# Performance work log

Hardware: AMD Instinct MI355X
Metric: run time of the kernel (lower is better)

The kernel has to match this reference:

```python
import jax, jax.numpy as jnp
import numpy as np

NL, H, PD, NH, NB = 4, 256, 64, 4, 65
B, L, AA = 2, 384, 48
DH = H // NH
MAX_REL = 32


def _ln(x, g, b):
    m = x.mean(-1, keepdims=True)
    v = ((x - m) ** 2).mean(-1, keepdims=True)
    return (x - m) * jax.lax.rsqrt(v + 1e-5) * g + b


def setup_inputs() -> dict:
    key = jax.random.key(0)
    ks = iter(jax.random.split(key, 64))
    w = lambda *s: jax.random.normal(next(ks), s, jnp.float32) * 0.02
    return dict(
        x=jax.random.normal(next(ks), (B, L, AA), jnp.float32),
        rp_w=w(AA, H), rp_b=jnp.zeros((H,), jnp.float32),
        pos_embed=w(L, H),
        pii_w=w(H, PD), pii_b=jnp.zeros((PD,), jnp.float32),
        pij_w=w(H, PD), pij_b=jnp.zeros((PD,), jnp.float32),
        rel_emb=w(2 * MAX_REL + 2, PD),
        ln_seq_g=jnp.ones((NL, H), jnp.float32), ln_seq_b=jnp.zeros((NL, H), jnp.float32),
        ln_pair_g=jnp.ones((NL, PD), jnp.float32), ln_pair_b=jnp.zeros((NL, PD), jnp.float32),
        pb_w=w(NL, PD, NH),
        in_w=w(NL, H, 3 * H), in_b=jnp.zeros((NL, 3 * H), jnp.float32),
        out_w=w(NL, H, H), out_b=jnp.zeros((NL, H), jnp.float32),
        ff_ln_g=jnp.ones((NL, H), jnp.float32), ff_ln_b=jnp.zeros((NL, H), jnp.float32),
        ff_w1=w(NL, H, 4 * H), ff_b1=jnp.zeros((NL, 4 * H), jnp.float32),
        ff_w2=w(NL, 4 * H, H), ff_b2=jnp.zeros((NL, H), jnp.float32),
        pu_ln_g=jnp.ones((NL, PD), jnp.float32), pu_ln_b=jnp.zeros((NL, PD), jnp.float32),
        pu_w1=w(NL, PD, PD), pu_b1=jnp.zeros((NL, PD), jnp.float32),
        pu_w2=w(NL, PD, PD), pu_b2=jnp.zeros((NL, PD), jnp.float32),
        outer_w=w(NL, 2 * H, PD), outer_b=jnp.zeros((NL, PD), jnp.float32),
        dh_ln_g=jnp.ones((PD,), jnp.float32), dh_ln_b=jnp.zeros((PD,), jnp.float32),
        dh_w1=w(PD, PD), dh_b1=jnp.zeros((PD,), jnp.float32),
        dh_w2=w(PD, NB), dh_b2=jnp.zeros((NB,), jnp.float32),
    )


def reference(x, rp_w, rp_b, pos_embed, pii_w, pii_b, pij_w, pij_b, rel_emb,
              ln_seq_g, ln_seq_b, ln_pair_g, ln_pair_b, pb_w, in_w, in_b,
              out_w, out_b, ff_ln_g, ff_ln_b, ff_w1, ff_b1, ff_w2, ff_b2,
              pu_ln_g, pu_ln_b, pu_w1, pu_b1, pu_w2, pu_b2, outer_w, outer_b,
              dh_ln_g, dh_ln_b, dh_w1, dh_b1, dh_w2, dh_b2):
    Bx, Lx, _ = x.shape
    gelu = lambda t: jax.nn.gelu(t, approximate=False)  # torch nn.GELU default (erf)
    h = x @ rp_w + rp_b + pos_embed[:Lx][None]
    # pair init: outer sum of two linear projections + clipped rel-pos embedding
    pair = (h @ pii_w + pii_b)[:, :, None, :] + (h @ pij_w + pij_b)[:, None, :, :]
    idx = jnp.arange(Lx)
    rel = jnp.clip(idx[None, :] - idx[:, None], -MAX_REL, MAX_REL) + MAX_REL  # (L,L)
    pair = pair + rel_emb[rel][None]
    for i in range(NL):
        seq_n = _ln(h, ln_seq_g[i], ln_seq_b[i])
        bias = _ln(pair, ln_pair_g[i], ln_pair_b[i]) @ pb_w[i]  # (B,L,L,NH)
        mask = bias.mean(axis=(0, 3))  # torch: permute->reshape(B*NH,L,L)->mean(0)
        qkv = seq_n @ in_w[i] + in_b[i]
        q, k, v = jnp.split(qkv, 3, axis=-1)
        q = q.reshape(Bx, Lx, NH, DH)
        k = k.reshape(Bx, Lx, NH, DH)
        v = v.reshape(Bx, Lx, NH, DH)
        scores = jnp.einsum('blhd,bmhd->bhlm', q, k) / float(np.sqrt(DH)) + mask
        attn = jax.nn.softmax(scores, axis=-1)
        o = jnp.einsum('bhlm,bmhd->blhd', attn, v).reshape(Bx, Lx, H)
        h = h + o @ out_w[i] + out_b[i]
        h = h + gelu(_ln(h, ff_ln_g[i], ff_ln_b[i]) @ ff_w1[i] + ff_b1[i]) @ ff_w2[i] + ff_b2[i]
        # outer_proj(cat([h_i, h_j])) == h@W[:H] outer-summed with h@W[H:]
        oi = h @ outer_w[i][:H]
        oj = h @ outer_w[i][H:]
        outer = oi[:, :, None, :] + oj[:, None, :, :] + outer_b[i]  # (B,L,L,PD)
        pair = pair + gelu(_ln(outer, pu_ln_g[i], pu_ln_b[i]) @ pu_w1[i] + pu_b1[i]) @ pu_w2[i] + pu_b2[i]
    logits = gelu(_ln(pair, dh_ln_g, dh_ln_b) @ dh_w1 + dh_b1) @ dh_w2 + dh_b2
    return (logits + jnp.swapaxes(logits, 1, 2)) / 2.0
```

## Files before the change

### kernel.cpp

```cpp
#include <hip/hip_runtime.h>
#include <math.h>

#define LSEQ 384
#define HD 256
#define PDIM 64
#define NHEAD 4
#define NBINS 65
#define BATCH 2
#define NTT (LSEQ / 16)
#define NTRI (NTT * (NTT + 1) / 2)

typedef __attribute__((ext_vector_type(8))) short bf16x8;
typedef __attribute__((ext_vector_type(16))) float f32x16;
typedef __attribute__((ext_vector_type(4))) float f32x4;
typedef __attribute__((ext_vector_type(4))) unsigned u32x4;
typedef __attribute__((ext_vector_type(4))) short s16x4;
#define MFMA32(a, b, c) __builtin_amdgcn_mfma_f32_32x32x16_bf16(a, b, c, 0, 0, 0)

template<int CTRL, int RMASK>
__device__ __forceinline__ float dpp_sum_step(float v) {
    int x = __builtin_amdgcn_update_dpp(0, __float_as_int(v), CTRL, RMASK, 0xf, true);
    return v + __int_as_float(x);
}
template<int CTRL, int RMASK>
__device__ __forceinline__ float dpp_max_step(float v) {
// ... 49 lines not shown
        float rb = b - __uint_as_float(hp & 0xffff0000u);
        h[j] = hp;
        l[j] = cvt_pk_bf(ra, rb);
    }
}
__device__ __forceinline__ bf16x8 as_bf(u32x4 x) {
    union { u32x4 u; bf16x8 b; } c; c.u = x; return c.b;
}
__device__ __forceinline__ bf16x8 ld8(const short* p) {
    s16x4 a = *(const s16x4*)p;
    s16x4 b = *(const s16x4*)(p + 4);
    bf16x8 r;
    r[0] = a[0]; r[1] = a[1]; r[2] = a[2]; r[3] = a[3];
    r[4] = b[0]; r[5] = b[1]; r[6] = b[2]; r[7] = b[3];
    return r;
}

__global__ void k_h_init(const float* __restrict__ x, const float* __restrict__ rp_w,
                         const float* __restrict__ rp_b, const float* __restrict__ pos,
                         float* __restrict__ h) {
    __shared__ float xs[48];
    int row = blockIdx.x;
    int l = row % LSEQ;
    int t = threadIdx.x;
    if (t < 48) xs[t] = x[row * 48 + t];
    __syncthreads();
    float acc = rp_b[t] + pos[l * HD + t];
#pragma unroll 8
    for (int a = 0; a < 48; ++a) acc += xs[a] * rp_w[a * HD + t];
    h[row * HD + t] = acc;
// ... 11 lines not shown
    __syncthreads();
    int col = t & 63;
    const float* w = (t < 64) ? wA : wB;
    const float* bias = (t < 64) ? bA : bB;
    float acc = bias ? bias[col] : 0.0f;
#pragma unroll 8
    for (int a = 0; a < HD; ++a) acc += hs[a] * w[a * PDIM + col];
    if (center) {
        float mean = wsum(acc) * (1.0f / PDIM);
        acc -= mean;
    }
    float* p = (t < 64) ? pA : pB;
    p[row * PDIM + col] = acc;
}

__global__ void __launch_bounds__(64) k_pair_init2(
    const float* __restrict__ pi, const float* __restrict__ pj,
    const float* __restrict__ rel_emb, const float* __restrict__ gpb,
    const float* __restrict__ cbv, float* __restrict__ pair,
    float* __restrict__ mask_out) {
    __shared__ __align__(16) float pt[32][65];
    int blk = blockIdx.x;
    int row = blk / 12, seg = blk % 12;
    int b = row / LSEQ, i = row % LSEQ;
    int t = threadIdx.x;
    int pl = t & 31, hq = t >> 5;
    int j0 = seg * 32;
    float piv = pi[row * 64 + t];
    const float* pjb = pj + ((size_t)b * LSEQ + j0) * 64;
#pragma unroll 8
    for (int j = 0; j < 32; ++j) {
        int r = j0 + j - i; r = r < -32 ? -32 : (r > 32 ? 32 : r); r += 32;
        pt[j][t] = piv + pjb[j * 64 + t] + rel_emb[r * 64 + t];
    }
    __syncthreads();
    float4* dst4 = (float4*)(pair + ((size_t)row * LSEQ + j0) * 64);
    for (int n = t; n < 512; n += 64) {
        int r2 = n >> 4, c4 = (n & 15) << 2;
        float4 g4 = { pt[r2][c4], pt[r2][c4 + 1], pt[r2][c4 + 2], pt[r2][c4 + 3] };
        dst4[n] = g4;
    }
    float vv[32];
    float sv = 0.0f;
#pragma unroll
    for (int c = 0; c < 32; ++c) { vv[c] = pt[pl][hq * 32 + c]; sv += vv[c]; }
    sv += __shfl_xor(sv, 32);
    float mean = sv * (1.0f / PDIM);
    float sd2 = 0.0f, sdg = 0.0f;
#pragma unroll
    for (int c = 0; c < 32; ++c) {
        float d = vv[c] - mean;
        sd2 = fmaf(d, d, sd2);
        sdg = fmaf(d, gpb[hq * 32 + c], sdg);
    }
    sd2 += __shfl_xor(sd2, 32);
    sdg += __shfl_xor(sdg, 32);
// ... 189 lines not shown
    if (lane == 0) red[4 + w] = ws;
    __syncthreads();
    float inv = 1.0f / (red[4] + red[5] + red[6] + red[7]);
    int d = t & 63, gq = t >> 6;
    float part = 0.0f;
    for (int m = gq * 96; m < (gq + 1) * 96; ++m)
        part += sc[m] * qkv[((size_t)(b * LSEQ + m)) * 768 + 512 + nh * 64 + d];
    op[gq][d] = part;
    __syncthreads();
    if (t < 64) {
        float ov = (op[0][t] + op[1][t] + op[2][t] + op[3][t]) * inv;
        o[((size_t)(b * LSEQ + l)) * HD + nh * 64 + t] = ov;
    }
}

template<bool DIST>
__global__ void __launch_bounds__(256) k_pair_upd(
    const float* __restrict__ ojc,
    const float* __restrict__ oic,
    const unsigned short* __restrict__ w1hT, const unsigned short* __restrict__ w1lT,
    const float* __restrict__ b1p,
    const unsigned short* __restrict__ w2hT, const unsigned short* __restrict__ w2lT,
    const float* __restrict__ b2, float* __restrict__ pair,
    const float* __restrict__ gpb, const float* __restrict__ cbv,
    float* __restrict__ mask_out,
    const unsigned short* __restrict__ dw1h, const unsigned short* __restrict__ dw1l,
    const float* __restrict__ db1p,
    const unsigned short* __restrict__ dw2h, const unsigned short* __restrict__ dw2l,
    const float* __restrict__ w2c, const float* __restrict__ db2,
    float* __restrict__ outg) {
    __shared__ __align__(16) char smem[DIST ? 33344 : 17472];
    short (*lw)[64][68] = (short (*)[64][68])smem;
    int blk = blockIdx.x;
    int row = blk / 3, seg = blk % 3;
    int b = row / LSEQ;
    int t = threadIdx.x;
    int wave = t >> 6, lane = t & 63;
    int pl = lane & 31, hq = lane >> 5;
    int jj = wave * 32 + pl;
    int p = seg * 128 + jj;
    const float* ojr = ojc + ((size_t)b * LSEQ + p) * 64;
    const float* oir = oic + (size_t)row * 64;
    float* prp = pair + ((size_t)row * LSEQ + p) * 64;

#define STAGE2(srcA, srcB) \
    for (int idx = t; idx < 2048; idx += 256) { \
        int rr2 = idx >> 5, cc2 = (idx & 31) * 2; \
        *(unsigned*)&lw[0][rr2][cc2] = *(const unsigned*)(srcA + rr2 * 64 + cc2); \
        *(unsigned*)&lw[1][rr2][cc2] = *(const unsigned*)(srcB + rr2 * 64 + cc2); \
    }

    float v[32];
    {
        const f32x4* a4 = (const f32x4*)ojr;
        const f32x4* c4 = (const f32x4*)oir;
#pragma unroll
        for (int s = 0; s < 4; ++s) {
            f32x4 a = a4[4 * s + 2 * hq], aa = a4[4 * s + 2 * hq + 1];
            f32x4 c = c4[4 * s + 2 * hq], cc = c4[4 * s + 2 * hq + 1];
#pragma unroll
            for (int j = 0; j < 4; ++j) {
                v[8 * s + j] = a[j] + c[j];
                v[8 * s + 4 + j] = aa[j] + cc[j];
            }
        }
    }
    STAGE2(w1hT, w1lT)

    float ss = 0.0f;
#pragma unroll
    for (int i = 0; i < 32; ++i) ss = fmaf(v[i], v[i], ss);
    ss += __shfl_xor(ss, 32);
    float rs = rsqrtf(ss * (1.0f / PDIM) + 1e-5f);
#pragma unroll
    for (int i = 0; i < 32; ++i) v[i] *= rs;
    u32x4 zh[4], zl[4];
#pragma unroll
    for (int s = 0; s < 4; ++s) pack8(v + 8 * s, zh[s], zl[s]);

    const f32x4* b14 = (const f32x4*)b1p;
    f32x4 bi0[4], bi1[4];
#pragma unroll
// ... 11 lines not shown
    for (int s = 0; s < 4; ++s) {
        int ko = 16 * s + 8 * hq;
        bf16x8 a0h = ld8(&lw[0][pl][ko]);
        bf16x8 a0l = ld8(&lw[1][pl][ko]);
        bf16x8 a1h = ld8(&lw[0][32 + pl][ko]);
        bf16x8 a1l = ld8(&lw[1][32 + pl][ko]);
        bf16x8 zhs = as_bf(zh[s]), zls = as_bf(zl[s]);
        acc0 = MFMA32(a0h, zhs, acc0);
        acc0 = MFMA32(a0h, zls, acc0);
        acc0 = MFMA32(a0l, zhs, acc0);
        acc1 = MFMA32(a1h, zhs, acc1);
        acc1 = MFMA32(a1h, zls, acc1);
        acc1 = MFMA32(a1l, zhs, acc1);
    }
    __syncthreads();
    STAGE2(w2hT, w2lT)

    float u0[16], u1[16];
#pragma unroll
    for (int r = 0; r < 16; ++r) { u0[r] = gelu_erf(acc0[r]); u1[r] = gelu_erf(acc1[r]); }

    f32x4 r0[4], r1[4], q0[4], q1[4];
    {
        const f32x4* pr4 = (const f32x4*)prp;
        const f32x4* b24 = (const f32x4*)b2;
#pragma unroll
        for (int g = 0; g < 4; ++g) {
            r0[g] = pr4[2 * g + hq];
            r1[g] = pr4[8 + 2 * g + hq];
            q0[g] = b24[2 * g + hq];
            q1[g] = b24[8 + 2 * g + hq];
        }
    }

    float rA0[4], rB0[4], rA1[4], rB1[4];
#pragma unroll
    for (int i = 0; i < 4; ++i) {
        rA0[i] = __shfl_xor(hq ? u0[i] : u0[4 + i], 32);
        rB0[i] = __shfl_xor(hq ? u0[8 + i] : u0[12 + i], 32);
        rA1[i] = __shfl_xor(hq ? u1[i] : u1[4 + i], 32);
        rB1[i] = __shfl_xor(hq ? u1[8 + i] : u1[12 + i], 32);
    }
    u32x4 uh[4], ul[4];
#pragma unroll
    for (int s = 0; s < 4; ++s) {
        int tt = s >> 1, q = s & 1;
// ... 22 lines not shown
    for (int s = 0; s < 4; ++s) {
        int ko = 16 * s + 8 * hq;
        bf16x8 a0h = ld8(&lw[0][pl][ko]);
        bf16x8 a0l = ld8(&lw[1][pl][ko]);
        bf16x8 a1h = ld8(&lw[0][32 + pl][ko]);
        bf16x8 a1l = ld8(&lw[1][32 + pl][ko]);
        bf16x8 uhs = as_bf(uh[s]), uls = as_bf(ul[s]);
        c0 = MFMA32(a0h, uhs, c0);
        c0 = MFMA32(a0h, uls, c0);
        c0 = MFMA32(a0l, uhs, c0);
        c1 = MFMA32(a1h, uhs, c1);
        c1 = MFMA32(a1h, uls, c1);
        c1 = MFMA32(a1l, uhs, c1);
    }

    if constexpr (!DIST) {
        const f32x4* gp4 = (const f32x4*)gpb;
        f32x4 gp0[4], gp1[4];
#pragma unroll
        for (int g = 0; g < 4; ++g) { gp0[g] = gp4[2 * g + hq]; gp1[g] = gp4[8 + 2 * g + hq]; }
        float sv = 0.0f;
#pragma unroll
        for (int r = 0; r < 16; ++r) sv += c0[r] + c1[r];
        sv += __shfl_xor(sv, 32);
        float mean = sv * (1.0f / PDIM);
        float sd2 = 0.0f, sdg = 0.0f;
#pragma unroll 4
        for (int r = 0; r < 16; ++r) {
            int g = r >> 2, i = r & 3;
            float d0 = c0[r] - mean, d1 = c1[r] - mean;
            sd2 = fmaf(d0, d0, sd2);
            sd2 = fmaf(d1, d1, sd2);
            sdg = fmaf(d0, gp0[g][i], sdg);
            sdg = fmaf(d1, gp1[g][i], sdg);
        }
        sd2 += __shfl_xor(sd2, 32);
        sdg += __shfl_xor(sdg, 32);
        float rsv = rsqrtf(sd2 * (1.0f / PDIM) + 1e-5f);
        float dot = rsv * sdg + cbv[0];
        if (hq == 0)
            atomicAdd(mask_out + (row % LSEQ) * LSEQ + p, dot * (1.0f / (BATCH * NHEAD)));
        f32x4* pw4 = (f32x4*)prp;
#pragma unroll
        for (int g = 0; g < 4; ++g) {
            f32x4 s0, s1;
#pragma unroll
            for (int i = 0; i < 4; ++i) { s0[i] = c0[4 * g + i]; s1[i] = c1[4 * g + i]; }
            pw4[2 * g + hq] = s0;
            pw4[8 + 2 * g + hq] = s1;
        }
    } else {
        float ra[4], rb[4], rc[4], rd[4];
#pragma unroll
        for (int i = 0; i < 4; ++i) {
            ra[i] = __shfl_xor(hq ? c0[i] : c0[4 + i], 32);
            rb[i] = __shfl_xor(hq ? c0[8 + i] : c0[12 + i], 32);
            rc[i] = __shfl_xor(hq ? c1[i] : c1[4 + i], 32);
            rd[i] = __shfl_xor(hq ? c1[8 + i] : c1[12 + i], 32);
        }
        float v2[32];
#pragma unroll
        for (int i = 0; i < 4; ++i) {
            v2[i]      = hq ? ra[i] : c0[i];
            v2[4 + i]  = hq ? c0[4 + i] : ra[i];
            v2[8 + i]  = hq ? rb[i] : c0[8 + i];
            v2[12 + i] = hq ? c0[12 + i] : rb[i];
            v2[16 + i] = hq ? rc[i] : c1[i];
            v2[20 + i] = hq ? c1[4 + i] : rc[i];
            v2[24 + i] = hq ? rd[i] : c1[8 + i];
            v2[28 + i] = hq ? c1[12 + i] : rd[i];
        }
        __syncthreads();
        STAGE2(dw1h, dw1l)

        float sm = 0.0f;
#pragma unroll
        for (int i = 0; i < 32; ++i) sm += v2[i];
        sm += __shfl_xor(sm, 32);
        float mean = sm * (1.0f / PDIM);
        float ss2 = 0.0f;
#pragma unroll
        for (int i = 0; i < 32; ++i) { v2[i] -= mean; ss2 = fmaf(v2[i], v2[i], ss2); }
        ss2 += __shfl_xor(ss2, 32);
        float rs2 = rsqrtf(ss2 * (1.0f / PDIM) + 1e-5f);
#pragma unroll
        for (int i = 0; i < 32; ++i) v2[i] *= rs2;
#pragma unroll
        for (int s = 0; s < 4; ++s) pack8(v2 + 8 * s, zh[s], zl[s]);

        const f32x4* d14 = (const f32x4*)db1p;
        const f32x4* d24 = (const f32x4*)db2;
        const f32x4* wc4 = (const f32x4*)w2c;
        f32x4 di0[4], di1[4], e0[4], e1[4], wc0[4], wc1[4];
#pragma unroll
        for (int g = 0; g < 4; ++g) {
            di0[g] = d14[2 * g + hq]; di1[g] = d14[8 + 2 * g + hq];
            e0[g] = d24[2 * g + hq];  e1[g] = d24[8 + 2 * g + hq];
            wc0[g] = wc4[2 * g + hq]; wc1[g] = wc4[8 + 2 * g + hq];
        }
        __syncthreads();

#pragma unroll
        for (int r = 0; r < 16; ++r) {
            acc0[r] = di0[r >> 2][r & 3];
            acc1[r] = di1[r >> 2][r & 3];
        }
#pragma unroll
        for (int s = 0; s < 4; ++s) {
            int ko = 16 * s + 8 * hq;
            bf16x8 a0h = ld8(&lw[0][pl][ko]);
            bf16x8 a0l = ld8(&lw[1][pl][ko]);
            bf16x8 a1h = ld8(&lw[0][32 + pl][ko]);
            bf16x8 a1l = ld8(&lw[1][32 + pl][ko]);
            bf16x8 zhs = as_bf(zh[s]), zls = as_bf(zl[s]);
            acc0 = MFMA32(a0h, zhs, acc0);
            acc0 = MFMA32(a0h, zls, acc0);
            acc0 = MFMA32(a0l, zhs, acc0);
            acc1 = MFMA32(a1h, zhs, acc1);
            acc1 = MFMA32(a1h, zls, acc1);
            acc1 = MFMA32(a1l, zhs, acc1);
        }
        __syncthreads();
        STAGE2(dw2h, dw2l)

        float p64 = 0.0f;
#pragma unroll
        for (int r = 0; r < 16; ++r) {
            int g = r >> 2, i = r & 3;
            u0[r] = gelu_erf(acc0[r]);
            u1[r] = gelu_erf(acc1[r]);
            p64 = fmaf(u0[r], wc0[g][i], p64);
            p64 = fmaf(u1[r], wc1[g][i], p64);
        }
        p64 += __shfl_xor(p64, 32);
#pragma unroll
        for (int i = 0; i < 4; ++i) {
            rA0[i] = __shfl_xor(hq ? u0[i] : u0[4 + i], 32);
            rB0[i] = __shfl_xor(hq ? u0[8 + i] : u0[12 + i], 32);
            rA1[i] = __shfl_xor(hq ? u1[i] : u1[4 + i], 32);
            rB1[i] = __shfl_xor(hq ? u1[8 + i] : u1[12 + i], 32);
        }
#pragma unroll
        for (int s = 0; s < 4; ++s) {
            int tt = s >> 1, q = s & 1;
            float fg[8];
#pragma unroll
            for (int i = 0; i < 4; ++i) {
                float own_f = q ? (tt ? u1[8 + i] : u0[8 + i]) : (tt ? u1[i] : u0[i]);
                float own_s = q ? (tt ? u1[12 + i] : u0[12 + i]) : (tt ? u1[4 + i] : u0[4 + i]);
                float rcv   = q ? (tt ? rB1[i] : rB0[i]) : (tt ? rA1[i] : rA0[i]);
                fg[i]     = hq ? rcv : own_f;
                fg[4 + i] = hq ? own_s : rcv;
            }
            pack8(fg, uh[s], ul[s]);
        }
        __syncthreads();

#pragma unroll
        for (int r = 0; r < 16; ++r) {
            c0[r] = e0[r >> 2][r & 3];
            c1[r] = e1[r >> 2][r & 3];
        }
#pragma unroll
        for (int s = 0; s < 4; ++s) {
            int ko = 16 * s + 8 * hq;
            bf16x8 a0h = ld8(&lw[0][pl][ko]);
            bf16x8 a0l = ld8(&lw[1][pl][ko]);
            bf16x8 a1h = ld8(&lw[0][32 + pl][ko]);
            bf16x8 a1l = ld8(&lw[1][32 + pl][ko]);
            bf16x8 uhs = as_bf(uh[s]), uls = as_bf(ul[s]);
            c0 = MFMA32(a0h, uhs, c0);
            c0 = MFMA32(a0h, uls, c0);
            c0 = MFMA32(a0l, uhs, c0);
            c1 = MFMA32(a1h, uhs, c1);
            c1 = MFMA32(a1h, uls, c1);
            c1 = MFMA32(a1l, uhs, c1);
        }
        __syncthreads();
        float (*pt)[65] = (float (*)[65])smem;
#pragma unroll
        for (int r = 0; r < 16; ++r) {
            int rr = (r & 3) + 8 * (r >> 2) + 4 * hq;
            pt[jj][rr] = c0[r];
            pt[jj][32 + rr] = c1[r];
        }
        if (hq == 0) pt[jj][64] = p64 + db2[64];
        __syncthreads();
        float4* dst = (float4*)(outg + ((size_t)row * LSEQ + seg * 128) * NBINS);
        const float4* srcl = (const float4*)&pt[0][0];
        for (int n = t; n < 128 * NBINS / 4; n += 256) dst[n] = srcl[n];
    }
#undef STAGE2
}

__global__ void k_sym(float* __restrict__ out) {
    int u = blockIdx.x;
    int b = 0;
    if (u >= NTRI) { b = 1; u -= NTRI; }
    int lt = 0, rem = NTT;
    while (u >= rem) { u -= rem; ++lt; --rem; }
    int mt = lt + u;
    int t = threadIdx.x;
    int g = t >> 6, lane = t & 63;
    float* ob = out + (size_t)b * LSEQ * LSEQ * NBINS;
    for (int e = g; e < 256; e += 4) {
        int i = e >> 4, j = e & 15;
        if (lt == mt && j < i) continue;
        size_t ia = ((size_t)(lt * 16 + i) * LSEQ + (mt * 16 + j)) * NBINS;
        size_t ib = ((size_t)(mt * 16 + j) * LSEQ + (lt * 16 + i)) * NBINS;
        for (int k = lane; k < NBINS; k += 64) {
            float a = ob[ia + k], c = ob[ib + k];
            float vv = 0.5f * (a + c);
            ob[ia + k] = vv;
            if (ia != ib) ob[ib + k] = vv;
        }
    }
}

extern "C" void kernel_launch(void* const* d_in, const int* in_sizes, int n_in,
                              void* d_out, int out_size, void* d_ws, size_t ws_size,
                              hipStream_t stream) {
    const float* x        = (const float*)d_in[0];
    const float* rp_w     = (const float*)d_in[1];
    const float* rp_b     = (const float*)d_in[2];
    const float* pos      = (const float*)d_in[3];
    const float* pii_w    = (const float*)d_in[4];
    const float* pii_b    = (const float*)d_in[5];
    const float* pij_w    = (const float*)d_in[6];
    const float* pij_b    = (const float*)d_in[7];
// ... 27 lines not shown
    const float* dh_b1    = (const float*)d_in[35];
    const float* dh_w2    = (const float*)d_in[36];
    const float* dh_b2    = (const float*)d_in[37];
    float* outp = (float*)d_out;

    float* W = (float*)d_ws;
    float* h    = W;  W += BATCH * LSEQ * HD;
    float* sn   = W;  W += BATCH * LSEQ * HD;
    float* qkv  = W;  W += BATCH * LSEQ * 3 * HD;
    float* ob   = W;  W += BATCH * LSEQ * HD;
    float* mid  = W;  W += BATCH * LSEQ * 4 * HD;
    float* maskA= W;  W += LSEQ * LSEQ;
    float* maskB= W;  W += LSEQ * LSEQ;
    float* poi  = W;  W += BATCH * LSEQ * PDIM;
    float* poj  = W;  W += BATCH * LSEQ * PDIM;
    float* b1p  = W;  W += 5 * 64;
    float* w2c  = W;  W += 64;
    float* gpb  = W;  W += 4 * 64;
    float* cbv  = W;  W += 64;
    unsigned short* w1hT = (unsigned short*)W;  W += 5 * 2048;
    unsigned short* w1lT = (unsigned short*)W;  W += 5 * 2048;
    unsigned short* w2hT = (unsigned short*)W;  W += 5 * 2048;
    unsigned short* w2lT = (unsigned short*)W;  W += 5 * 2048;
    unsigned short* qwT_h = (unsigned short*)W;  W += 4 * 196608 / 2;
    unsigned short* qwT_l = (unsigned short*)W;  W += 4 * 196608 / 2;
    unsigned short* owT_h = (unsigned short*)W;  W += 4 * 65536 / 2;
    unsigned short* owT_l = (unsigned short*)W;  W += 4 * 65536 / 2;
    unsigned short* f1T_h = (unsigned short*)W;  W += 4 * 262144 / 2;
    unsigned short* f1T_l = (unsigned short*)W;  W += 4 * 262144 / 2;
    unsigned short* f2T_h = (unsigned short*)W;  W += 4 * 262144 / 2;
    unsigned short* f2T_l = (unsigned short*)W;  W += 4 * 262144 / 2;
    float* pair = W;  W += (size_t)BATCH * LSEQ * LSEQ * PDIM;

    const int rows = BATCH * LSEQ;

    k_prep<<<5, 64, 0, stream>>>(pu_ln_g, pu_ln_b, pu_w1, pu_b1, pu_w2,
                                 dh_ln_g, dh_ln_b, dh_w1, dh_b1, dh_w2,
                                 w1hT, w1lT, w2hT, w2lT, b1p, w2c);
    k_maskprep<<<4, 64, 0, stream>>>(ln_pair_g, ln_pair_b, pb_w, gpb, cbv);
    k_split_T<<<4 * 4 * 12, 256, 0, stream>>>(in_w,  qwT_h, qwT_l, 256, 768,  4, 12, 196608, 196608);
    k_split_T<<<4 * 4 * 4,  256, 0, stream>>>(out_w, owT_h, owT_l, 256, 256,  4, 4,  65536,  65536);
    k_split_T<<<4 * 4 * 16, 256, 0, stream>>>(ff_w1, f1T_h, f1T_l, 256, 1024, 4, 16, 262144, 262144);
    k_split_T<<<4 * 16 * 4, 256, 0, stream>>>(ff_w2, f2T_h, f2T_l, 1024, 256, 16, 4, 262144, 262144);
    k_h_init<<<rows, 256, 0, stream>>>(x, rp_w, rp_b, pos, h);
    k_proj2<<<rows, 128, 0, stream>>>(h, pii_w, pij_w, pii_b, pij_b, 0, poi, poj);
    hipMemsetAsync(maskA, 0, LSEQ * LSEQ * sizeof(float), stream);
    k_pair_init2<<<rows * 12, 64, 0, stream>>>(poi, poj, rel_emb, gpb, cbv, pair, maskA);

    float* mcur = maskA;
    float* mnext = maskB;
    for (int i = 0; i < 4; ++i) {
        k_ln_seq<<<rows, 256, 0, stream>>>(h, ln_seq_g + i * HD, ln_seq_b + i * HD, sn);
        k_gemm<false><<<576, 64, 0, stream>>>(sn, qwT_h + i * 196608, qwT_l + i * 196608,
                                              in_b + i * 768, nullptr, qkv, 256, 768);
        k_attn<<<BATCH * NHEAD * LSEQ, 256, 0, stream>>>(qkv, mcur, ob);
        k_gemm<false><<<192, 64, 0, stream>>>(ob, owT_h + i * 65536, owT_l + i * 65536,
                                              out_b + i * 256, h, h, 256, 256);
        k_ln_seq<<<rows, 256, 0, stream>>>(h, ff_ln_g + i * HD, ff_ln_b + i * HD, sn);
        k_gemm<true><<<768, 64, 0, stream>>>(sn, f1T_h + i * 262144, f1T_l + i * 262144,
                                             ff_b1 + i * 1024, nullptr, mid, 256, 1024);
        k_gemm<false><<<192, 64, 0, stream>>>(mid, f2T_h + i * 262144, f2T_l + i * 262144,
                                              ff_b2 + i * 256, h, h, 1024, 256);
        k_proj2<<<rows, 128, 0, stream>>>(h, outer_w + i * 2 * HD * PDIM,
                                          outer_w + i * 2 * HD * PDIM + HD * PDIM,
                                          outer_b + i * PDIM, nullptr, 1, poi, poj);
        if (i < 3) {
            hipMemsetAsync(mnext, 0, LSEQ * LSEQ * sizeof(float), stream);
            k_pair_upd<false><<<rows * 3, 256, 0, stream>>>(
                poj, poi,
                w1hT + i * 4096, w1lT + i * 4096, b1p + i * 64,
                w2hT + i * 4096, w2lT + i * 4096, pu_b2 + i * PDIM, pair,
                gpb + (i + 1) * 64, cbv + (i + 1), mnext,
                nullptr, nullptr, nullptr, nullptr, nullptr, nullptr, nullptr, nullptr);
            float* tmp = mcur; mcur = mnext; mnext = tmp;
        } else {
            k_pair_upd<true><<<rows * 3, 256, 0, stream>>>(
                poj, poi,
                w1hT + 3 * 4096, w1lT + 3 * 4096, b1p + 3 * 64,
                w2hT + 3 * 4096, w2lT + 3 * 4096, pu_b2 + 3 * PDIM, pair,
                nullptr, nullptr, nullptr,
                w1hT + 4 * 4096, w1lT + 4 * 4096, b1p + 4 * 64,
                w2hT + 4 * 4096, w2lT + 4 * 4096, w2c, dh_b2, outp);
        }
    }

    k_sym<<<2 * NTRI, 256, 0, stream>>>(outp);
}
```

Before: 1.050 ms.

## Fuse pair init into first update and symmetrize inside final distance kernel

The initial pair tensor is no longer written by the init kernel. The first pair-update pass rebuilds it on the fly from the projections and relative embeddings, so one full pair write and read is skipped. The last layer's update and distance head move into a new kernel that computes each (i,j) and (j,i) cell pair together, averages them, and writes both transposed output tiles. This removes the separate symmetrization kernel and its read-modify-write over the output, but doubles per-block MLP work for the final layer and uses a triangular tile mapping with scattered writes.

```diff
diff --git a/kernel.cpp b/kernel.cpp
--- a/kernel.cpp
+++ b/kernel.cpp
@@ -7,8 +7,6 @@
 #define NHEAD 4
 #define NBINS 65
 #define BATCH 2
-#define NTT (LSEQ / 16)
-#define NTRI (NTT * (NTT + 1) / 2)
 
 typedef __attribute__((ext_vector_type(8))) short bf16x8;
 typedef __attribute__((ext_vector_type(16))) float f32x16;
@@ -88,6 +86,16 @@
     r[0] = a[0]; r[1] = a[1]; r[2] = a[2]; r[3] = a[3];
     r[4] = b[0]; r[5] = b[1]; r[6] = b[2]; r[7] = b[3];
     return r;
+}
+
+__device__ __forceinline__ void stage_w(short (*lw)[64][68], int t,
+                                        const unsigned short* __restrict__ srcA,
+                                        const unsigned short* __restrict__ srcB) {
+    for (int idx = t; idx < 2048; idx += 256) {
+        int rr2 = idx >> 5, cc2 = (idx & 31) * 2;
+        *(unsigned*)&lw[0][rr2][cc2] = *(const unsigned*)(srcA + rr2 * 64 + cc2);
+        *(unsigned*)&lw[1][rr2][cc2] = *(const unsigned*)(srcB + rr2 * 64 + cc2);
+    }
 }
 
 __global__ void k_h_init(const float* __restrict__ x, const float* __restrict__ rp_w,
@@ -129,11 +137,10 @@
     p[row * PDIM + col] = acc;
 }
 
-__global__ void __launch_bounds__(64) k_pair_init2(
+__global__ void __launch_bounds__(64) k_mask0(
     const float* __restrict__ pi, const float* __restrict__ pj,
     const float* __restrict__ rel_emb, const float* __restrict__ gpb,
-    const float* __restrict__ cbv, float* __restrict__ pair,
-    float* __restrict__ mask_out) {
+    const float* __restrict__ cbv, float* __restrict__ mask_out) {
     __shared__ __align__(16) float pt[32][65];
     int blk = blockIdx.x;
     int row = blk / 12, seg = blk % 12;
@@ -149,12 +156,6 @@
         pt[j][t] = piv + pjb[j * 64 + t] + rel_emb[r * 64 + t];
     }
     __syncthreads();
-    float4* dst4 = (float4*)(pair + ((size_t)row * LSEQ + j0) * 64);
-    for (int n = t; n < 512; n += 64) {
-        int r2 = n >> 4, c4 = (n & 15) << 2;
-        float4 g4 = { pt[r2][c4], pt[r2][c4 + 1], pt[r2][c4 + 2], pt[r2][c4 + 3] };
-        dst4[n] = g4;
-    }
     float vv[32];
     float sv = 0.0f;
 #pragma unroll
@@ -374,7 +375,7 @@
     }
 }
 
-template<bool DIST>
+template<bool INIT>
 __global__ void __launch_bounds__(256) k_pair_upd(
     const float* __restrict__ ojc,
     const float* __restrict__ oic,
@@ -384,12 +385,9 @@
     const float* __restrict__ b2, float* __restrict__ pair,
     const float* __restrict__ gpb, const float* __restrict__ cbv,
     float* __restrict__ mask_out,
-    const unsigned short* __restrict__ dw1h, const unsigned short* __restrict__ dw1l,
-    const float* __restrict__ db1p,
-    const unsigned short* __restrict__ dw2h, const unsigned short* __restrict__ dw2l,
-    const float* __restrict__ w2c, const float* __restrict__ db2,
-    float* __restrict__ outg) {
-    __shared__ __align__(16) char smem[DIST ? 33344 : 17472];
+    const float* __restrict__ ipi, const float* __restrict__ ipj,
+    const float* __restrict__ rel) {
+    __shared__ __align__(16) char smem[17472];
     short (*lw)[64][68] = (short (*)[64][68])smem;
     int blk = blockIdx.x;
     int row = blk / 3, seg = blk % 3;
@@ -403,13 +401,6 @@
     const float* oir = oic + (size_t)row * 64;
     float* prp = pair + ((size_t)row * LSEQ + p) * 64;
 
-#define STAGE2(srcA, srcB) \
-    for (int idx = t; idx < 2048; idx += 256) { \
-        int rr2 = idx >> 5, cc2 = (idx & 31) * 2; \
-        *(unsigned*)&lw[0][rr2][cc2] = *(const unsigned*)(srcA + rr2 * 64 + cc2); \
-        *(unsigned*)&lw[1][rr2][cc2] = *(const unsigned*)(srcB + rr2 * 64 + cc2); \
-    }
-
     float v[32];
     {
         const f32x4* a4 = (const f32x4*)ojr;
@@ -425,7 +416,7 @@
             }
         }
     }
-    STAGE2(w1hT, w1lT)
+    stage_w(lw, t, w1hT, w1lT);
 
     float ss = 0.0f;
 #pragma unroll
@@ -467,7 +458,7 @@
         acc1 = MFMA32(a1l, zhs, acc1);
     }
     __syncthreads();
-    STAGE2(w2hT, w2lT)
+    stage_w(lw, t, w2hT, w2lT);
 
     float u0[16], u1[16];
 #pragma unroll
@@ -475,14 +466,29 @@
 
     f32x4 r0[4], r1[4], q0[4], q1[4];
     {
-        const f32x4* pr4 = (const f32x4*)prp;
         const f32x4* b24 = (const f32x4*)b2;
-#pragma unroll
-        for (int g = 0; g < 4; ++g) {
-            r0[g] = pr4[2 * g + hq];
-            r1[g] = pr4[8 + 2 * g + hq];
-            q0[g] = b24[2 * g + hq];
-            q1[g] = b24[8 + 2 * g + hq];
+        if constexpr (INIT) {
+            int l = row % LSEQ;
+            int rr_ = p - l; rr_ = rr_ < -32 ? -32 : (rr_ > 32 ? 32 : rr_); rr_ += 32;
+            const f32x4* i4 = (const f32x4*)(ipi + (size_t)row * 64);
+            const f32x4* j4 = (const f32x4*)(ipj + ((size_t)b * LSEQ + p) * 64);
+            const f32x4* e4 = (const f32x4*)(rel + rr_ * 64);
+#pragma unroll
+            for (int g = 0; g < 4; ++g) {
+                r0[g] = i4[2 * g + hq] + j4[2 * g + hq] + e4[2 * g + hq];
+                r1[g] = i4[8 + 2 * g + hq] + j4[8 + 2 * g + hq] + e4[8 + 2 * g + hq];
+                q0[g] = b24[2 * g + hq];
+                q1[g] = b24[8 + 2 * g + hq];
+            }
+        } else {
+            const f32x4* pr4 = (const f32x4*)prp;
+#pragma unroll
+            for (int g = 0; g < 4; ++g) {
+                r0[g] = pr4[2 * g + hq];
+                r1[g] = pr4[8 + 2 * g + hq];
+                q0[g] = b24[2 * g + hq];
+                q1[g] = b24[8 + 2 * g + hq];
+            }
         }
     }
 
@@ -535,7 +541,7 @@
         c1 = MFMA32(a1l, uhs, c1);
     }
 
-    if constexpr (!DIST) {
+    {
         const f32x4* gp4 = (const f32x4*)gpb;
         f32x4 gp0[4], gp1[4];
 #pragma unroll
@@ -561,179 +567,344 @@
         float dot = rsv * sdg + cbv[0];
         if (hq == 0)
             atomicAdd(mask_out + (row % LSEQ) * LSEQ + p, dot * (1.0f / (BATCH * NHEAD)));
-        f32x4* pw4 = (f32x4*)prp;
+    }
+    f32x4* pw4 = (f32x4*)prp;
+#pragma unroll
+    for (int g = 0; g < 4; ++g) {
+        f32x4 s0, s1;
+#pragma unroll
+        for (int i = 0; i < 4; ++i) { s0[i] = c0[4 * g + i]; s1[i] = c1[4 * g + i]; }
+        pw4[2 * g + hq] = s0;
+        pw4[8 + 2 * g + hq] = s1;
+    }
+}
+
+__device__ __forceinline__ void dist_cell(
+    int t, int pl, int hq,
+    const float* __restrict__ oiR, const float* __restrict__ ojC,
+    const float* __restrict__ prp, short (*lw)[64][68],
+    const unsigned short* __restrict__ w1hT, const unsigned short* __restrict__ w1lT,
+    const float* __restrict__ b1p,
+    const unsigned short* __restrict__ w2hT, const unsigned short* __restrict__ w2lT,
+    const float* __restrict__ b2,
+    const unsigned short* __restrict__ dw1h, const unsigned short* __restrict__ dw1l,
+    const float* __restrict__ db1p,
+    const unsigned short* __restrict__ dw2h, const unsigned short* __restrict__ dw2l,
+    const float* __restrict__ w2c, const float* __restrict__ db2,
+    f32x16& c0o, f32x16& c1o, float& p64o) {
+    __syncthreads();
+    float v[32];
+    {
+        const f32x4* a4 = (const f32x4*)ojC;
+        const f32x4* c4 = (const f32x4*)oiR;
+#pragma unroll
+        for (int s = 0; s < 4; ++s) {
+            f32x4 a = a4[4 * s + 2 * hq], aa = a4[4 * s + 2 * hq + 1];
+            f32x4 c = c4[4 * s + 2 * hq], cc = c4[4 * s + 2 * hq + 1];
+#pragma unroll
+            for (int j = 0; j < 4; ++j) {
+                v[8 * s + j] = a[j] + c[j];
+                v[8 * s + 4 + j] = aa[j] + cc[j];
+            }
+        }
+    }
+    stage_w(lw, t, w1hT, w1lT);
+    float ss = 0.0f;
+#pragma unroll
+    for (int i = 0; i < 32; ++i) ss = fmaf(v[i], v[i], ss);
+    ss += __shfl_xor(ss, 32);
+    float rs = rsqrtf(ss * (1.0f / PDIM) + 1e-5f);
+#pragma unroll
+    for (int i = 0; i < 32; ++i) v[i] *= rs;
+    u32x4 zh[4], zl[4];
+#pragma unroll
+    for (int s = 0; s < 4; ++s) pack8(v + 8 * s, zh[s], zl[s]);
+    const f32x4* b14 = (const f32x4*)b1p;
+    f32x4 bi0[4], bi1[4];
+#pragma unroll
+    for (int g = 0; g < 4; ++g) { bi0[g] = b14[2 * g + hq]; bi1[g] = b14[8 + 2 * g + hq]; }
+    __syncthreads();
+    f32x16 acc0, acc1;
+#pragma unroll
+    for (int r = 0; r < 16; ++r) { acc0[r] = bi0[r >> 2][r & 3]; acc1[r] = bi1[r >> 2][r & 3]; }
+#pragma unroll
+    for (int s = 0; s < 4; ++s) {
+        int ko = 16 * s + 8 * hq;
+        bf16x8 a0h = ld8(&lw[0][pl][ko]);
+        bf16x8 a0l = ld8(&lw[1][pl][ko]);
+        bf16x8 a1h = ld8(&lw[0][32 + pl][ko]);
+        bf16x8 a1l = ld8(&lw[1][32 + pl][ko]);
+        bf16x8 zhs = as_bf(zh[s]), zls = as_bf(zl[s]);
+        acc0 = MFMA32(a0h, zhs, acc0);
+        acc0 = MFMA32(a0h, zls, acc0);
+        acc0 = MFMA32(a0l, zhs, acc0);
+        acc1 = MFMA32(a1h, zhs, acc1);
+        acc1 = MFMA32(a1h, zls, acc1);
+        acc1 = MFMA32(a1l, zhs, acc1);
+    }
+    __syncthreads();
+    stage_w(lw, t, w2hT, w2lT);
+    float u0[16], u1[16];
+#pragma unroll
+    for (int r = 0; r < 16; ++r) { u0[r] = gelu_erf(acc0[r]); u1[r] = gelu_erf(acc1[r]); }
+    f32x4 r0[4], r1[4], q0[4], q1[4];
+    {
+        const f32x4* pr4 = (const f32x4*)prp;
+        const f32x4* b24 = (const f32x4*)b2;
 #pragma unroll
         for (int g = 0; g < 4; ++g) {
-            f32x4 s0, s1;
-#pragma unroll
-            for (int i = 0; i < 4; ++i) { s0[i] = c0[4 * g + i]; s1[i] = c1[4 * g + i]; }
-            pw4[2 * g + hq] = s0;
-            pw4[8 + 2 * g + hq] = s1;
-        }
-    } else {
-        float ra[4], rb[4], rc[4], rd[4];
+            r0[g] = pr4[2 * g + hq];
+            r1[g] = pr4[8 + 2 * g + hq];
+            q0[g] = b24[2 * g + hq];
+            q1[g] = b24[8 + 2 * g + hq];
+        }
+    }
+    float rA0[4], rB0[4], rA1[4], rB1[4];
+#pragma unroll
+    for (int i = 0; i < 4; ++i) {
+        rA0[i] = __shfl_xor(hq ? u0[i] : u0[4 + i], 32);
+        rB0[i] = __shfl_xor(hq ? u0[8 + i] : u0[12 + i], 32);
+        rA1[i] = __shfl_xor(hq ? u1[i] : u1[4 + i], 32);
+        rB1[i] = __shfl_xor(hq ? u1[8 + i] : u1[12 + i], 32);
+    }
+    u32x4 uh[4], ul[4];
+#pragma unroll
+    for (int s = 0; s < 4; ++s) {
+        int tt = s >> 1, q = s & 1;
+        float fg[8];
 #pragma unroll
         for (int i = 0; i < 4; ++i) {
-            ra[i] = __shfl_xor(hq ? c0[i] : c0[4 + i], 32);
-            rb[i] = __shfl_xor(hq ? c0[8 + i] : c0[12 + i], 32);
-            rc[i] = __shfl_xor(hq ? c1[i] : c1[4 + i], 32);
-            rd[i] = __shfl_xor(hq ? c1[8 + i] : c1[12 + i], 32);
-        }
-        float v2[32];
+            float own_f = q ? (tt ? u1[8 + i] : u0[8 + i]) : (tt ? u1[i] : u0[i]);
+            float own_s = q ? (tt ? u1[12 + i] : u0[12 + i]) : (tt ? u1[4 + i] : u0[4 + i]);
+            float rcv   = q ? (tt ? rB1[i] : rB0[i]) : (tt ? rA1[i] : rA0[i]);
+            fg[i]     = hq ? rcv : own_f;
+            fg[4 + i] = hq ? own_s : rcv;
+        }
+        pack8(fg, uh[s], ul[s]);
+    }
+    __syncthreads();
+    f32x16 c0, c1;
+#pragma unroll
+    for (int r = 0; r < 16; ++r) {
+        int g = r >> 2, i = r & 3;
+        c0[r] = q0[g][i] + r0[g][i];
+        c1[r] = q1[g][i] + r1[g][i];
+    }
+#pragma unroll
+    for (int s = 0; s < 4; ++s) {
+        int ko = 16 * s + 8 * hq;
+        bf16x8 a0h = ld8(&lw[0][pl][ko]);
+        bf16x8 a0l = ld8(&lw[1][pl][ko]);
+        bf16x8 a1h = ld8(&lw[0][32 + pl][ko]);
+        bf16x8 a1l = ld8(&lw[1][32 + pl][ko]);
+        bf16x8 uhs = as_bf(uh[s]), uls = as_bf(ul[s]);
+        c0 = MFMA32(a0h, uhs, c0);
+        c0 = MFMA32(a0h, uls, c0);
+        c0 = MFMA32(a0l, uhs, c0);
+        c1 = MFMA32(a1h, uhs, c1);
+        c1 = MFMA32(a1h, uls, c1);
+        c1 = MFMA32(a1l, uhs, c1);
+    }
+    float ra[4], rb[4], rc[4], rd[4];
+#pragma unroll
+    for (int i = 0; i < 4; ++i) {
+        ra[i] = __shfl_xor(hq ? c0[i] : c0[4 + i], 32);
+        rb[i] = __shfl_xor(hq ? c0[8 + i] : c0[12 + i], 32);
+        rc[i] = __shfl_xor(hq ? c1[i] : c1[4 + i], 32);
+        rd[i] = __shfl_xor(hq ? c1[8 + i] : c1[12 + i], 32);
+    }
+    float v2[32];
+#pragma unroll
+    for (int i = 0; i < 4; ++i) {
+        v2[i]      = hq ? ra[i] : c0[i];
+        v2[4 + i]  = hq ? c0[4 + i] : ra[i];
+        v2[8 + i]  = hq ? rb[i] : c0[8 + i];
+        v2[12 + i] = hq ? c0[12 + i] : rb[i];
+        v2[16 + i] = hq ? rc[i] : c1[i];
+        v2[20 + i] = hq ? c1[4 + i] : rc[i];
+        v2[24 + i] = hq ? rd[i] : c1[8 + i];
+        v2[28 + i] = hq ? c1[12 + i] : rd[i];
+    }
+    __syncthreads();
+    stage_w(lw, t, dw1h, dw1l);
+    float sm = 0.0f;
+#pragma unroll
+    for (int i = 0; i < 32; ++i) sm += v2[i];
+    sm += __shfl_xor(sm, 32);
+    float mean = sm * (1.0f / PDIM);
+    float ss2 = 0.0f;
+#pragma unroll
+    for (int i = 0; i < 32; ++i) { v2[i] -= mean; ss2 = fmaf(v2[i], v2[i], ss2); }
+    ss2 += __shfl_xor(ss2, 32);
+    float rs2 = rsqrtf(ss2 * (1.0f / PDIM) + 1e-5f);
+#pragma unroll
+    for (int i = 0; i < 32; ++i) v2[i] *= rs2;
+#pragma unroll
+    for (int s = 0; s < 4; ++s) pack8(v2 + 8 * s, zh[s], zl[s]);
+    const f32x4* d14 = (const f32x4*)db1p;
+    const f32x4* d24 = (const f32x4*)db2;
+    const f32x4* wc4 = (const f32x4*)w2c;
+    f32x4 di0[4], di1[4], e0[4], e1[4], wc0[4], wc1[4];
+#pragma unroll
+    for (int g = 0; g < 4; ++g) {
+        di0[g] = d14[2 * g + hq]; di1[g] = d14[8 + 2 * g + hq];
+        e0[g] = d24[2 * g + hq];  e1[g] = d24[8 + 2 * g + hq];
+        wc0[g] = wc4[2 * g + hq]; wc1[g] = wc4[8 + 2 * g + hq];
+    }
+    __syncthreads();
+#pragma unroll
+    for (int r = 0; r < 16; ++r) { acc0[r] = di0[r >> 2][r & 3]; acc1[r] = di1[r >> 2][r & 3]; }
+#pragma unroll
+    for (int s = 0; s < 4; ++s) {
+        int ko = 16 * s + 8 * hq;
+        bf16x8 a0h = ld8(&lw[0][pl][ko]);
+        bf16x8 a0l = ld8(&lw[1][pl][ko]);
+        bf16x8 a1h = ld8(&lw[0][32 + pl][ko]);
+        bf16x8 a1l = ld8(&lw[1][32 + pl][ko]);
+        bf16x8 zhs = as_bf(zh[s]), zls = as_bf(zl[s]);
+        acc0 = MFMA32(a0h, zhs, acc0);
+        acc0 = MFMA32(a0h, zls, acc0);
+        acc0 = MFMA32(a0l, zhs, acc0);
+        acc1 = MFMA32(a1h, zhs, acc1);
+        acc1 = MFMA32(a1h, zls, acc1);
+        acc1 = MFMA32(a1l, zhs, acc1);
+    }
+    __syncthreads();
+    stage_w(lw, t, dw2h, dw2l);
+    float p64 = 0.0f;
+#pragma unroll
+    for (int r = 0; r < 16; ++r) {
+        int g = r >> 2, i = r & 3;
+        u0[r] = gelu_erf(acc0[r]);
+        u1[r] = gelu_erf(acc1[r]);
+        p64 = fmaf(u0[r], wc0[g][i], p64);
+        p64 = fmaf(u1[r], wc1[g][i], p64);
+    }
+    p64 += __shfl_xor(p64, 32);
+#pragma unroll
+    for (int i = 0; i < 4; ++i) {
+        rA0[i] = __shfl_xor(hq ? u0[i] : u0[4 + i], 32);
+        rB0[i] = __shfl_xor(hq ? u0[8 + i] : u0[12 + i], 32);
+        rA1[i] = __shfl_xor(hq ? u1[i] : u1[4 + i], 32);
+        rB1[i] = __shfl_xor(hq ? u1[8 + i] : u1[12 + i], 32);
+    }
+#pragma unroll
+    for (int s = 0; s < 4; ++s) {
+        int tt = s >> 1, q = s & 1;
+        float fg[8];
 #pragma unroll
         for (int i = 0; i < 4; ++i) {
-            v2[i]      = hq ? ra[i] : c0[i];
-            v2[4 + i]  = hq ? c0[4 + i] : ra[i];
-            v2[8 + i]  = hq ? rb[i] : c0[8 + i];
-            v2[12 + i] = hq ? c0[12 + i] : rb[i];
-            v2[16 + i] = hq ? rc[i] : c1[i];
-            v2[20 + i] = hq ? c1[4 + i] : rc[i];
-            v2[24 + i] = hq ? rd[i] : c1[8 + i];
-            v2[28 + i] = hq ? c1[12 + i] : rd[i];
-        }
-        __syncthreads();
-        STAGE2(dw1h, dw1l)
-
-        float sm = 0.0f;
-#pragma unroll
-        for (int i = 0; i < 32; ++i) sm += v2[i];
-        sm += __shfl_xor(sm, 32);
-        float mean = sm * (1.0f / PDIM);
-        float ss2 = 0.0f;
-#pragma unroll
-        for (int i = 0; i < 32; ++i) { v2[i] -= mean; ss2 = fmaf(v2[i], v2[i], ss2); }
-        ss2 += __shfl_xor(ss2, 32);
-        float rs2 = rsqrtf(ss2 * (1.0f / PDIM) + 1e-5f);
-#pragma unroll
-        for (int i = 0; i < 32; ++i) v2[i] *= rs2;
-#pragma unroll
-        for (int s = 0; s < 4; ++s) pack8(v2 + 8 * s, zh[s], zl[s]);
-
-        const f32x4* d14 = (const f32x4*)db1p;
-        const f32x4* d24 = (const f32x4*)db2;
-        const f32x4* wc4 = (const f32x4*)w2c;
-        f32x4 di0[4], di1[4], e0[4], e1[4], wc0[4], wc1[4];
-#pragma unroll
-        for (int g = 0; g < 4; ++g) {
-            di0[g] = d14[2 * g + hq]; di1[g] = d14[8 + 2 * g + hq];
-            e0[g] = d24[2 * g + hq];  e1[g] = d24[8 + 2 * g + hq];
-            wc0[g] = wc4[2 * g + hq]; wc1[g] = wc4[8 + 2 * g + hq];
-        }
-        __syncthreads();
-
-#pragma unroll
-        for (int r = 0; r < 16; ++r) {
-            acc0[r] = di0[r >> 2][r & 3];
-            acc1[r] = di1[r >> 2][r & 3];
-        }
-#pragma unroll
-        for (int s = 0; s < 4; ++s) {
-            int ko = 16 * s + 8 * hq;
-            bf16x8 a0h = ld8(&lw[0][pl][ko]);
-            bf16x8 a0l = ld8(&lw[1][pl][ko]);
-            bf16x8 a1h = ld8(&lw[0][32 + pl][ko]);
-            bf16x8 a1l = ld8(&lw[1][32 + pl][ko]);
-            bf16x8 zhs = as_bf(zh[s]), zls = as_bf(zl[s]);
-            acc0 = MFMA32(a0h, zhs, acc0);
-            acc0 = MFMA32(a0h, zls, acc0);
-            acc0 = MFMA32(a0l, zhs, acc0);
-            acc1 = MFMA32(a1h, zhs, acc1);
-            acc1 = MFMA32(a1h, zls, acc1);
-            acc1 = MFMA32(a1l, zhs, acc1);
-        }
-        __syncthreads();
-        STAGE2(dw2h, dw2l)
-
-        float p64 = 0.0f;
-#pragma unroll
-        for (int r = 0; r < 16; ++r) {
-            int g = r >> 2, i = r & 3;
-            u0[r] = gelu_erf(acc0[r]);
-            u1[r] = gelu_erf(acc1[r]);
-            p64 = fmaf(u0[r], wc0[g][i], p64);
-            p64 = fmaf(u1[r], wc1[g][i], p64);
-        }
-        p64 += __shfl_xor(p64, 32);
-#pragma unroll
-        for (int i = 0; i < 4; ++i) {
-            rA0[i] = __shfl_xor(hq ? u0[i] : u0[4 + i], 32);
-            rB0[i] = __shfl_xor(hq ? u0[8 + i] : u0[12 + i], 32);
-            rA1[i] = __shfl_xor(hq ? u1[i] : u1[4 + i], 32);
-            rB1[i] = __shfl_xor(hq ? u1[8 + i] : u1[12 + i], 32);
-        }
-#pragma unroll
-        for (int s = 0; s < 4; ++s) {
-            int tt = s >> 1, q = s & 1;
-            float fg[8];
-#pragma unroll
-            for (int i = 0; i < 4; ++i) {
-                float own_f = q ? (tt ? u1[8 + i] : u0[8 + i]) : (tt ? u1[i] : u0[i]);
-                float own_s = q ? (tt ? u1[12 + i] : u0[12 + i]) : (tt ? u1[4 + i] : u0[4 + i]);
-                float rcv   = q ? (tt ? rB1[i] : rB0[i]) : (tt ? rA1[i] : rA0[i]);
-                fg[i]     = hq ? rcv : own_f;
-                fg[4 + i] = hq ? own_s : rcv;
-            }
-            pack8(fg, uh[s], ul[s]);
-        }
-        __syncthreads();
-
-#pragma unroll
-        for (int r = 0; r < 16; ++r) {
-            c0[r] = e0[r >> 2][r & 3];
-            c1[r] = e1[r >> 2][r & 3];
-        }
-#pragma unroll
-        for (int s = 0; s < 4; ++s) {
-            int ko = 16 * s + 8 * hq;
-            bf16x8 a0h = ld8(&lw[0][pl][ko]);
-            bf16x8 a0l = ld8(&lw[1][pl][ko]);
-            bf16x8 a1h = ld8(&lw[0][32 + pl][ko]);
-            bf16x8 a1l = ld8(&lw[1][32 + pl][ko]);
-            bf16x8 uhs = as_bf(uh[s]), uls = as_bf(ul[s]);
-            c0 = MFMA32(a0h, uhs, c0);
-            c0 = MFMA32(a0h, uls, c0);
-            c0 = MFMA32(a0l, uhs, c0);
-            c1 = MFMA32(a1h, uhs, c1);
-            c1 = MFMA32(a1h, uls, c1);
-            c1 = MFMA32(a1l, uhs, c1);
-        }
-        __syncthreads();
-        float (*pt)[65] = (float (*)[65])smem;
+            float own_f = q ? (tt ? u1[8 + i] : u0[8 + i]) : (tt ? u1[i] : u0[i]);
+            float own_s = q ? (tt ? u1[12 + i] : u0[12 + i]) : (tt ? u1[4 + i] : u0[4 + i]);
+            float rcv   = q ? (tt ? rB1[i] : rB0[i]) : (tt ? rA1[i] : rA0[i]);
+            fg[i]     = hq ? rcv : own_f;
+            fg[4 + i] = hq ? own_s : rcv;
+        }
+        pack8(fg, uh[s], ul[s]);
+    }
+    __syncthreads();
+#pragma unroll
+    for (int r = 0; r < 16; ++r) { c0[r] = e0[r >> 2][r & 3]; c1[r] = e1[r >> 2][r & 3]; }
+#pragma unroll
+    for (int s = 0; s < 4; ++s) {
+        int ko = 16 * s + 8 * hq;
+        bf16x8 a0h = ld8(&lw[0][pl][ko]);
+        bf16x8 a0l = ld8(&lw[1][pl][ko]);
+        bf16x8 a1h = ld8(&lw[0][32 + pl][ko]);
+        bf16x8 a1l = ld8(&lw[1][32 + pl][ko]);
+        bf16x8 uhs = as_bf(uh[s]), uls = as_bf(ul[s]);
+        c0 = MFMA32(a0h, uhs, c0);
+        c0 = MFMA32(a0h, uls, c0);
+        c0 = MFMA32(a0l, uhs, c0);
+        c1 = MFMA32(a1h, uhs, c1);
+        c1 = MFMA32(a1h, uls, c1);
+        c1 = MFMA32(a1l, uhs, c1);
+    }
+    c0o = c0; c1o = c1; p64o = p64;
+}
+
+__global__ void __launch_bounds__(256) k_pair_dist(
+    const float* __restrict__ ojc, const float* __restrict__ oic,
+    const float* __restrict__ pair,
+    const unsigned short* __restrict__ w1hT, const unsigned short* __restrict__ w1lT,
+    const float* __restrict__ b1p,
+    const unsigned short* __restrict__ w2hT, const unsigned short* __restrict__ w2lT,
+    const float* __restrict__ b2,
+    const unsigned short* __restrict__ dw1h, const unsigned short* __restrict__ dw1l,
+    const float* __restrict__ db1p,
+    const unsigned short* __restrict__ dw2h, const unsigned short* __restrict__ dw2l,
+    const float* __restrict__ w2c, const float* __restrict__ db2,
+    float* __restrict__ outg) {
+    __shared__ __align__(16) char smem[33344];
+    short (*lw)[64][68] = (short (*)[64][68])smem;
+    int t = threadIdx.x;
+    int wave = t >> 6, lane = t & 63;
+    int pl = lane & 31, hq = lane >> 5;
+    int blk = blockIdx.x;
+    int b = blk / 624;
+    int rem = blk % 624;
+    int pr = rem >> 3, strip = rem & 7;
+    int lt = 0;
+    { int r = 12; while (pr >= r) { pr -= r; --r; ++lt; } }
+    int jt = lt + pr;
+    int rowA = lt * 32 + strip * 4 + wave;
+    int colA = jt * 32 + pl;
+    size_t ia = (size_t)b * LSEQ + rowA;
+    size_t ja = (size_t)b * LSEQ + colA;
+
+    f32x16 cA0, cA1, cB0, cB1;
+    float pA, pB;
+    dist_cell(t, pl, hq, oic + ia * 64, ojc + ja * 64,
+              pair + (ia * LSEQ + colA) * 64, lw,
+              w1hT, w1lT, b1p, w2hT, w2lT, b2,
+              dw1h, dw1l, db1p, dw2h, dw2l, w2c, db2, cA0, cA1, pA);
+    dist_cell(t, pl, hq, oic + ja * 64, ojc + ia * 64,
+              pair + (ja * LSEQ + rowA) * 64, lw,
+              w1hT, w1lT, b1p, w2hT, w2lT, b2,
+              dw1h, dw1l, db1p, dw2h, dw2l, w2c, db2, cB0, cB1, pB);
+#pragma unroll
+    for (int r = 0; r < 16; ++r) {
+        cA0[r] = 0.5f * (cA0[r] + cB0[r]);
+        cA1[r] = 0.5f * (cA1[r] + cB1[r]);
+    }
+    float pav = 0.5f * (pA + pB) + db2[64];
+
+    __syncthreads();
+    {
+        float (*ptA)[32][NBINS] = (float (*)[32][NBINS])smem;
 #pragma unroll
         for (int r = 0; r < 16; ++r) {
             int rr = (r & 3) + 8 * (r >> 2) + 4 * hq;
-            pt[jj][rr] = c0[r];
-            pt[jj][32 + rr] = c1[r];
-        }
-        if (hq == 0) pt[jj][64] = p64 + db2[64];
+            ptA[wave][pl][rr] = cA0[r];
+            ptA[wave][pl][32 + rr] = cA1[r];
+        }
+        if (hq == 0) ptA[wave][pl][64] = pav;
         __syncthreads();
-        float4* dst = (float4*)(outg + ((size_t)row * LSEQ + seg * 128) * NBINS);
-        const float4* srcl = (const float4*)&pt[0][0];
-        for (int n = t; n < 128 * NBINS / 4; n += 256) dst[n] = srcl[n];
-    }
-#undef STAGE2
-}
-
-__global__ void k_sym(float* __restrict__ out) {
-    int u = blockIdx.x;
-    int b = 0;
-    if (u >= NTRI) { b = 1; u -= NTRI; }
-    int lt = 0, rem = NTT;
-    while (u >= rem) { u -= rem; ++lt; --rem; }
-    int mt = lt + u;
-    int t = threadIdx.x;
-    int g = t >> 6, lane = t & 63;
-    float* ob = out + (size_t)b * LSEQ * LSEQ * NBINS;
-    for (int e = g; e < 256; e += 4) {
-        int i = e >> 4, j = e & 15;
-        if (lt == mt && j < i) continue;
-        size_t ia = ((size_t)(lt * 16 + i) * LSEQ + (mt * 16 + j)) * NBINS;
-        size_t ib = ((size_t)(mt * 16 + j) * LSEQ + (lt * 16 + i)) * NBINS;
-        for (int k = lane; k < NBINS; k += 64) {
-            float a = ob[ia + k], c = ob[ib + k];
-            float vv = 0.5f * (a + c);
-            ob[ia + k] = vv;
-            if (ia != ib) ob[ib + k] = vv;
+        const float4* s4 = (const float4*)smem;
+        for (int n = t; n < 4 * 520; n += 256) {
+            int rw = n / 520, ix = n % 520;
+            float4* d4 = (float4*)(outg +
+                (((size_t)b * LSEQ + lt * 32 + strip * 4 + rw) * LSEQ + jt * 32) * NBINS);
+            d4[ix] = s4[n];
+        }
+    }
+    __syncthreads();
+    {
+        float (*ptB)[4][NBINS] = (float (*)[4][NBINS])smem;
+#pragma unroll
+        for (int r = 0; r < 16; ++r) {
+            int rr = (r & 3) + 8 * (r >> 2) + 4 * hq;
+            ptB[pl][wave][rr] = cA0[r];
+            ptB[pl][wave][32 + rr] = cA1[r];
+        }
+        if (hq == 0) ptB[pl][wave][64] = pav;
+        __syncthreads();
+        const float4* s4 = (const float4*)smem;
+        for (int n = t; n < 32 * 65; n += 256) {
+            int rw = n / 65, ix = n % 65;
+            float4* d4 = (float4*)(outg +
+                (((size_t)b * LSEQ + jt * 32 + rw) * LSEQ + lt * 32 + strip * 4) * NBINS);
+            d4[ix] = s4[n];
         }
     }
 }
@@ -791,6 +962,8 @@
     float* maskB= W;  W += LSEQ * LSEQ;
     float* poi  = W;  W += BATCH * LSEQ * PDIM;
     float* poj  = W;  W += BATCH * LSEQ * PDIM;
+    float* poi0 = W;  W += BATCH * LSEQ * PDIM;
+    float* poj0 = W;  W += BATCH * LSEQ * PDIM;
     float* b1p  = W;  W += 5 * 64;
     float* w2c  = W;  W += 64;
     float* gpb  = W;  W += 4 * 64;
@@ -820,9 +993,9 @@
     k_split_T<<<4 * 4 * 16, 256, 0, stream>>>(ff_w1, f1T_h, f1T_l, 256, 1024, 4, 16, 262144, 262144);
     k_split_T<<<4 * 16 * 4, 256, 0, stream>>>(ff_w2, f2T_h, f2T_l, 1024, 256, 16, 4, 262144, 262144);
     k_h_init<<<rows, 256, 0, stream>>>(x, rp_w, rp_b, pos, h);
-    k_proj2<<<rows, 128, 0, stream>>>(h, pii_w, pij_w, pii_b, pij_b, 0, poi, poj);
+    k_proj2<<<rows, 128, 0, stream>>>(h, pii_w, pij_w, pii_b, pij_b, 0, poi0, poj0);
     hipMemsetAsync(maskA, 0, LSEQ * LSEQ * sizeof(float), stream);
-    k_pair_init2<<<rows * 12, 64, 0, stream>>>(poi, poj, rel_emb, gpb, cbv, pair, maskA);
+    k_mask0<<<rows * 12, 64, 0, stream>>>(poi0, poj0, rel_emb, gpb, cbv, maskA);
 
     float* mcur = maskA;
     float* mnext = maskB;
@@ -841,25 +1014,29 @@
         k_proj2<<<rows, 128, 0, stream>>>(h, outer_w + i * 2 * HD * PDIM,
                                           outer_w + i * 2 * HD * PDIM + HD * PDIM,
                                           outer_b + i * PDIM, nullptr, 1, poi, poj);
-        if (i < 3) {
+        if (i == 0) {
+            hipMemsetAsync(mnext, 0, LSEQ * LSEQ * sizeof(float), stream);
+            k_pair_upd<true><<<rows * 3, 256, 0, stream>>>(
+                poj, poi,
+                w1hT, w1lT, b1p, w2hT, w2lT, pu_b2, pair,
+                gpb + 64, cbv + 1, mnext, poi0, poj0, rel_emb);
+            float* tmp = mcur; mcur = mnext; mnext = tmp;
+        } else if (i < 3) {
             hipMemsetAsync(mnext, 0, LSEQ * LSEQ * sizeof(float), stream);
             k_pair_upd<false><<<rows * 3, 256, 0, stream>>>(
                 poj, poi,
                 w1hT + i * 4096, w1lT + i * 4096, b1p + i * 64,
                 w2hT + i * 4096, w2lT + i * 4096, pu_b2 + i * PDIM, pair,
                 gpb + (i + 1) * 64, cbv + (i + 1), mnext,
-                nullptr, nullptr, nullptr, nullptr, nullptr, nullptr, nullptr, nullptr);
+                nullptr, nullptr, nullptr);
             float* tmp = mcur; mcur = mnext; mnext = tmp;
         } else {
-            k_pair_upd<true><<<rows * 3, 256, 0, stream>>>(
-                poj, poi,
+            k_pair_dist<<<BATCH * 78 * 8, 256, 0, stream>>>(
+                poj, poi, pair,
                 w1hT + 3 * 4096, w1lT + 3 * 4096, b1p + 3 * 64,
-                w2hT + 3 * 4096, w2lT + 3 * 4096, pu_b2 + 3 * PDIM, pair,
-                nullptr, nullptr, nullptr,
+                w2hT + 3 * 4096, w2lT + 3 * 4096, pu_b2 + 3 * PDIM,
                 w1hT + 4 * 4096, w1lT + 4 * 4096, b1p + 4 * 64,
                 w2hT + 4 * 4096, w2lT + 4 * 4096, w2c, dh_b2, outp);
         }
     }
-
-    k_sym<<<2 * NTRI, 256, 0, stream>>>(outp);
-}
+}
```

Measured after the change: 1.088 ms. +3.6%, slower.
